# Performance work log

Measured on AMD Instinct MI355X. Metric: run time of the kernel, lower is better.

The kernel has to match this reference:

```python
import jax, jax.numpy as jnp
import numpy as np

N, E, D, H = 50000, 800000, 64, 64  # nodes, edges, in_dim, hid_dim


def setup_inputs() -> dict:
    key = jax.random.key(0)
    ks = jax.random.split(key, 16)
    s = lambda fan_in: 1.0 / np.sqrt(fan_in)
    inp = {
        "node_feat": jax.random.normal(ks[0], (N, D), jnp.float32),
        "coord": jax.random.normal(ks[1], (N, 3), jnp.float32),
        "edge_list": jax.random.randint(ks[2], (E, 2), 0, N, jnp.int32),
        # edge_mlp: Linear(2D+1 -> H), Linear(H -> H)
        "We1": jax.random.normal(ks[3], (2 * D + 1, H), jnp.float32) * s(2 * D + 1),
        "be1": jnp.zeros((H,), jnp.float32),
        "We2": jax.random.normal(ks[4], (H, H), jnp.float32) * s(H),
        "be2": jnp.zeros((H,), jnp.float32),
        # node_mlp: Linear(H+D -> H), Linear(H -> H)
        "Wn1": jax.random.normal(ks[5], (H + D, H), jnp.float32) * s(H + D),
        "bn1": jnp.zeros((H,), jnp.float32),
        "Wn2": jax.random.normal(ks[6], (H, H), jnp.float32) * s(H),
        "bn2": jnp.zeros((H,), jnp.float32),
        # coord_mlp: Linear(H -> H), Linear(H -> 1, bias=False, xavier gain 1e-3)
        "Wc1": jax.random.normal(ks[7], (H, H), jnp.float32) * s(H),
        "bc1": jnp.zeros((H,), jnp.float32),
        "wc": jax.random.normal(ks[8], (H, 1), jnp.float32) * 0.001,
    }
    return inp


def reference(node_feat, coord, edge_list, We1, be1, We2, be2,
              Wn1, bn1, Wn2, bn2, Wc1, bc1, wc):
    n = node_feat.shape[0]
    node_in = edge_list[:, 0]
    node_out = edge_list[:, 1]

    # coord2radial (normalize=False)
    coord_diff = coord[node_out] - coord[node_in]            # [E,3]
    radial = jnp.sum(coord_diff * coord_diff, axis=1, keepdims=True)  # [E,1]

    # edge_function (no edge_attr, no attention)
    edge_in = jnp.concatenate(
        [node_feat[node_in], node_feat[node_out], radial], axis=1)    # [E,2D+1]
    h = jax.nn.relu(edge_in @ We1 + be1)
    edge_feat = jax.nn.relu(h @ We2 + be2)                   # [E,H]

    # coord_function, coords_agg='mean'
    trans_w = jax.nn.relu(edge_feat @ Wc1 + bc1) @ wc        # [E,1]
    weighted_trans = coord_diff * trans_w                    # [E,3]
    agg = jax.ops.segment_sum(weighted_trans, node_out, num_segments=n)
    cnt = jax.ops.segment_sum(jnp.ones((node_out.shape[0],), coord.dtype),
                              node_out, num_segments=n)
    coord_out = coord + agg / jnp.maximum(cnt, 1.0)[:, None]

    # node_function (residual, dims match)
    agg_edge = jax.ops.segment_sum(edge_feat, node_out, num_segments=n)  # [N,H]
    node_in_feat = jnp.concatenate([node_feat, agg_edge], axis=1)
    nf = jax.nn.relu(node_in_feat @ Wn1 + bn1) @ Wn2 + bn2
    node_feat_out = node_feat + nf

    return node_feat_out, coord_out
```

## Files before the change

kernel.cpp:

```cpp
#include <hip/hip_runtime.h>

#define NN 50000
#define NE 800000
#define PREP_BLOCKS 784
#define PREP_THREADS (PREP_BLOCKS * 256)

typedef __bf16 bf16x8 __attribute__((ext_vector_type(8)));
typedef float  f32x4  __attribute__((ext_vector_type(4)));

__device__ __forceinline__ float frelu(float x) { return fmaxf(x, 0.f); }

__global__ __launch_bounds__(256) void prep_kernel(
    const float* __restrict__ nf, const int* __restrict__ el,
    const float* __restrict__ We1, const float* __restrict__ We2,
    const float* __restrict__ Wc1, const float* __restrict__ Wn1,
    const float* __restrict__ Wn2, const float* __restrict__ be1,
    __bf16* __restrict__ W2T,  __bf16* __restrict__ Wc1T,
    __bf16* __restrict__ Wn1T, __bf16* __restrict__ Wn2T,
    __bf16* __restrict__ Pa, __bf16* __restrict__ Pb,
    int* __restrict__ deg, int* __restrict__ rank, float* __restrict__ agg_edge,
    int* __restrict__ counter)
{
    __shared__ __align__(16) __bf16 w1lds[64 * 128];
    if (blockIdx.x < 196) {
        for (int idx = threadIdx.x; idx < 64 * 128; idx += 256) {
            const int k = idx >> 6;
            const int j = idx & 63;
            w1lds[j * 128 + (k ^ ((j & 7) << 3))] = (__bf16)We1[k * 64 + j];
        }
    }

    const int tid = blockIdx.x * 256 + threadIdx.x;
    if (tid == 0) *counter = 0;

    if (tid < 4096) {
        const int j = tid & 63, k = tid >> 6;
        W2T [j * 64 + k] = (__bf16)We2[k * 64 + j];
        Wc1T[j * 64 + k] = (__bf16)Wc1[k * 64 + j];
        Wn2T[j * 64 + k] = (__bf16)Wn2[k * 64 + j];
        Wn1T[j * 128 + k]      = (__bf16)Wn1[k * 64 + j];
        Wn1T[j * 128 + 64 + k] = (__bf16)Wn1[(64 + k) * 64 + j];
    }

    {
        const f32x4 z = (f32x4){0.f, 0.f, 0.f, 0.f};
        for (int i = tid; i < NN * 16; i += PREP_THREADS)
            ((f32x4*)agg_edge)[i] = z;
    }

    for (int e = tid; e < NE; e += PREP_THREADS) {
        const int2 pr = ((const int2*)el)[e];
        rank[e] = atomicAdd(&deg[pr.y], 1);
    }

    if (blockIdx.x >= 196) return;
    __syncthreads();

    const int w = threadIdx.x >> 6, lane = threadIdx.x & 63;
    const int c = lane & 15, g = lane >> 4;
    const int mbase = blockIdx.x * 256 + w * 64;

    bf16x8 af[4][2];
#pragma unroll
    for (int m = 0; m < 4; ++m) {
        int node = mbase + m * 16 + c;
        node = (node < NN) ? node : (NN - 1);
#pragma unroll
        for (int s = 0; s < 2; ++s) {
            const int k0 = s * 32 + g * 8;
            const float4 v0 = *(const float4*)(nf + (size_t)node * 64 + k0);
            const float4 v1 = *(const float4*)(nf + (size_t)node * 64 + k0 + 4);
            bf16x8 a;
            a[0] = (__bf16)v0.x; a[1] = (__bf16)v0.y; a[2] = (__bf16)v0.z; a[3] = (__bf16)v0.w;
            a[4] = (__bf16)v1.x; a[5] = (__bf16)v1.y; a[6] = (__bf16)v1.z; a[7] = (__bf16)v1.w;
            af[m][s] = a;
        }
    }

    {
        f32x4 cc[4][4];
#pragma unroll
        for (int m = 0; m < 4; ++m)
#pragma unroll
            for (int n = 0; n < 4; ++n) cc[m][n] = (f32x4){0.f, 0.f, 0.f, 0.f};
#pragma unroll
        for (int n = 0; n < 4; ++n)
#pragma unroll
            for (int s = 0; s < 2; ++s) {
                const int j = n * 16 + c;
                const bf16x8 b = *(const bf16x8*)&w1lds[j * 128 + ((s * 32 + g * 8) ^ ((j & 7) << 3))];
#pragma unroll
                for (int m = 0; m < 4; ++m)
                    cc[m][n] = __builtin_amdgcn_mfma_f32_16x16x32_bf16(af[m][s], b, cc[m][n], 0, 0, 0);
            }
#pragma unroll
        for (int m = 0; m < 4; ++m)
#pragma unroll
            for (int n = 0; n < 4; ++n)
#pragma unroll
                for (int r = 0; r < 4; ++r) {
                    const int node = mbase + m * 16 + g * 4 + r;
                    if (node < NN) Pa[(size_t)node * 64 + n * 16 + c] = (__bf16)cc[m][n][r];
                }
    }
    {
        f32x4 cc[4][4];
#pragma unroll
        for (int m = 0; m < 4; ++m)
#pragma unroll
            for (int n = 0; n < 4; ++n) cc[m][n] = (f32x4){0.f, 0.f, 0.f, 0.f};
#pragma unroll
        for (int n = 0; n < 4; ++n)
#pragma unroll
            for (int s = 0; s < 2; ++s) {
                const int j = n * 16 + c;
                const bf16x8 b = *(const bf16x8*)&w1lds[j * 128 + 64 + ((s * 32 + g * 8) ^ ((j & 7) << 3))];
#pragma unroll
                for (int m = 0; m < 4; ++m)
                    cc[m][n] = __builtin_amdgcn_mfma_f32_16x16x32_bf16(af[m][s], b, cc[m][n], 0, 0, 0);
            }
#pragma unroll
        for (int n = 0; n < 4; ++n) {
            const float bb = be1[n * 16 + c];
#pragma unroll
            for (int m = 0; m < 4; ++m)
#pragma unroll
                for (int r = 0; r < 4; ++r) {
                    const int node = mbase + m * 16 + g * 4 + r;
                    if (node < NN) Pb[(size_t)node * 64 + n * 16 + c] = (__bf16)(cc[m][n][r] + bb);
                }
        }
    }
}

__global__ __launch_bounds__(256) void alloc_kernel(
    const int* __restrict__ deg, int* __restrict__ base, int* __restrict__ counter)
{
    const int n = blockIdx.x * 256 + threadIdx.x;
    const int lid = threadIdx.x & 63;
    const int d = (n < NN) ? deg[n] : 0;
    int pre = d;
#pragma unroll
    for (int off = 1; off < 64; off <<= 1) {
        const int v = __shfl_up(pre, off);
        if (lid >= off) pre += v;
    }
    const int excl = pre - d;
    const int tot = __shfl(pre, 63);
    int wbase = 0;
    if (lid == 63) wbase = atomicAdd(counter, tot);
    wbase = __shfl(wbase, 63);
    if (n < NN) base[n] = wbase + excl;
}

__global__ __launch_bounds__(256) void scatter_kernel(
    const int* __restrict__ el, const int* __restrict__ base,
    const int* __restrict__ rank, int2* __restrict__ sorted_el,
    float* __restrict__ agg3)
{
    const int e = blockIdx.x * 256 + threadIdx.x;
    if (e < NN * 3) agg3[e] = 0.f;
    const int2 pr = ((const int2*)el)[e];
    sorted_el[base[pr.y] + rank[e]] = pr;
}

__global__ __launch_bounds__(256, 5) void edge_mfma(
    const __bf16* __restrict__ Pa, const __bf16* __restrict__ Pb,
    const float* __restrict__ coord, const int2* __restrict__ sorted_el,
    const float* __restrict__ We1,
    const __bf16* __restrict__ W2T, const float* __restrict__ be2,
    const __bf16* __restrict__ Wc1T, const float* __restrict__ bc1,
    const float* __restrict__ wc,
    float* __restrict__ agg_edge, float* __restrict__ agg3)
{
    __shared__ __align__(16) __bf16 tile[4][64 * 32];
    __shared__ int   nin_s[4][64];
    __shared__ int   nout_s[4][64];
    __shared__ float rad_s[4][64];
    __shared__ float tw_s[4][64];
    __shared__ float cd_s[4][64][3];

    const int w    = threadIdx.x >> 6;
    const int lane = threadIdx.x & 63;
    const int c    = lane & 15;
    const int g    = lane >> 4;
    const int ebase = blockIdx.x * 256 + w * 64;

    const int2 pr = sorted_el[ebase + lane];
    const int nin = pr.x, nout = pr.y;
    nin_s[w][lane]  = nin;
    nout_s[w][lane] = nout;
    const float cdx = coord[3 * nout + 0] - coord[3 * nin + 0];
    const float cdy = coord[3 * nout + 1] - coord[3 * nin + 1];
    const float cdz = coord[3 * nout + 2] - coord[3 * nin + 2];
    rad_s[w][lane] = cdx * cdx + cdy * cdy + cdz * cdz;
    cd_s[w][lane][0] = cdx; cd_s[w][lane][1] = cdy; cd_s[w][lane][2] = cdz;

    bf16x8 af[4][2];
#pragma unroll
    for (int s = 0; s < 2; ++s) {
        const int k0 = s * 32 + g * 8;
        const float4 w1a = *(const float4*)(We1 + 128 * 64 + k0);
        const float4 w1b = *(const float4*)(We1 + 128 * 64 + k0 + 4);
        float wv[8] = {w1a.x, w1a.y, w1a.z, w1a.w, w1b.x, w1b.y, w1b.z, w1b.w};
#pragma unroll
        for (int m = 0; m < 4; ++m) {
            const int e  = m * 16 + c;
            const int ni = nin_s[w][e];
            const int no = nout_s[w][e];
            const float rad = rad_s[w][e];
            const bf16x8 pa = *(const bf16x8*)(Pa + (size_t)ni * 64 + k0);
            const bf16x8 pb = *(const bf16x8*)(Pb + (size_t)no * 64 + k0);
            bf16x8 a;
#pragma unroll
            for (int i = 0; i < 8; ++i)
                a[i] = (__bf16)frelu((float)pa[i] + (float)pb[i] + rad * wv[i]);
            af[m][s] = a;
        }
    }

    bf16x8 a2[4][2];
#pragma unroll
    for (int p = 0; p < 2; ++p) {
        f32x4 c1h[4][2];
#pragma unroll
        for (int q = 0; q < 2; ++q) {
            const float b = be2[(2 * p + q) * 16 + c];
#pragma unroll
            for (int m = 0; m < 4; ++m) c1h[m][q] = (f32x4){b, b, b, b};
        }
#pragma unroll
        for (int q = 0; q < 2; ++q)
#pragma unroll
            for (int s = 0; s < 2; ++s) {
                const bf16x8 b = *(const bf16x8*)(W2T + ((2 * p + q) * 16 + c) * 64 + s * 32 + g * 8);
#pragma unroll
                for (int m = 0; m < 4; ++m)
                    c1h[m][q] = __builtin_amdgcn_mfma_f32_16x16x32_bf16(af[m][s], b, c1h[m][q], 0, 0, 0);
            }

#pragma unroll
        for (int m = 0; m < 4; ++m)
#pragma unroll
            for (int q = 0; q < 2; ++q)
#pragma unroll
                for (int r = 0; r < 4; ++r) {
                    const int e = m * 16 + g * 4 + r;
                    const int lc = q * 16 + c;
                    tile[w][e * 32 + (lc ^ (((e >> 1) & 3) << 3))] = (__bf16)frelu(c1h[m][q][r]);
                }

#pragma unroll
        for (int m = 0; m < 4; ++m) {
            const int e = m * 16 + c;
            a2[m][p] = *(const bf16x8*)&tile[w][e * 32 + ((g * 8) ^ (((e >> 1) & 3) << 3))];
        }

        {
            const int lc = lane & 31;
            const int rbase = (lane >> 5) * 32;
            int cur = nout_s[w][rbase];
            float acc = 0.f;
#pragma unroll 4
            for (int rr = 0; rr < 32; ++rr) {
                const int r = rbase + rr;
                acc += (float)tile[w][r * 32 + (lc ^ (((r >> 1) & 3) << 3))];
                const int nxt = (rr < 31) ? nout_s[w][r + 1] : -1;
                if (nxt != cur) {
                    atomicAdd(&agg_edge[(size_t)cur * 64 + p * 32 + lc], acc);
                    acc = 0.f;
                    cur = nxt;
                }
            }
        }
    }

    f32x4 twp[4];
#pragma unroll
    for (int m = 0; m < 4; ++m) twp[m] = (f32x4){0.f, 0.f, 0.f, 0.f};
#pragma unroll
    for (int n = 0; n < 4; ++n) {
        const float b = bc1[n * 16 + c];
        const float wn = wc[n * 16 + c];
        f32x4 c2[4];
#pragma unroll
        for (int m = 0; m < 4; ++m) c2[m] = (f32x4){b, b, b, b};
#pragma unroll
        for (int s = 0; s < 2; ++s) {
            const bf16x8 bb = *(const bf16x8*)(Wc1T + (n * 16 + c) * 64 + s * 32 + g * 8);
#pragma unroll
            for (int m = 0; m < 4; ++m)
                c2[m] = __builtin_amdgcn_mfma_f32_16x16x32_bf16(a2[m][s], bb, c2[m], 0, 0, 0);
        }
#pragma unroll
        for (int m = 0; m < 4; ++m)
#pragma unroll
            for (int r = 0; r < 4; ++r)
                twp[m][r] = fmaf(frelu(c2[m][r]), wn, twp[m][r]);
    }

#pragma unroll
    for (int m = 0; m < 4; ++m) {
#pragma unroll
        for (int r = 0; r < 4; ++r) {
            float p = twp[m][r];
            p += __shfl_xor(p, 1);
            p += __shfl_xor(p, 2);
            p += __shfl_xor(p, 4);
            p += __shfl_xor(p, 8);
            if (c == 0) tw_s[w][m * 16 + g * 4 + r] = p;
        }
    }

    if (lane < 48) {
        const int dim = lane % 3, chunk = lane / 3;
        const int r0 = chunk * 4;
        int cur = nout_s[w][r0];
        float acc = 0.f;
#pragma unroll
        for (int rr = 0; rr < 4; ++rr) {
            const int r = r0 + rr;
            acc += cd_s[w][r][dim] * tw_s[w][r];
            const int nxt = (rr < 3) ? nout_s[w][r + 1] : -1;
            if (nxt != cur) {
                atomicAdd(&agg3[3 * cur + dim], acc);
                acc = 0.f;
                cur = nxt;
            }
        }
    }
}

__global__ __launch_bounds__(256) void node_mfma(
    const float* __restrict__ nf, const float* __restrict__ coord,
    const float* __restrict__ agg_edge, const int* __restrict__ deg,
    float* agg3_coordout,
    const __bf16* __restrict__ Wn1T, const float* __restrict__ bn1,
    const __bf16* __restrict__ Wn2T, const float* __restrict__ bn2,
    float* __restrict__ out_feat)
{
    __shared__ __align__(16) __bf16 tile[4][64 * 64];
    const int t = threadIdx.x;
    const int w = t >> 6, lane = t & 63, c = lane & 15, g = lane >> 4;
    const int nblk = blockIdx.x * 256;

    const int nodeT = nblk + t;
    if (nodeT < NN) {
        const float invc = 1.f / fmaxf((float)deg[nodeT], 1.f);
#pragma unroll
        for (int d = 0; d < 3; ++d) {
            const float a = agg3_coordout[3 * nodeT + d];
            agg3_coordout[3 * nodeT + d] = coord[3 * nodeT + d] + a * invc;
        }
    }

    const int mbase = nblk + w * 64;

    bf16x8 a1[4][4];
#pragma unroll
    for (int m = 0; m < 4; ++m) {
        int node = mbase + m * 16 + c;
        node = (node < NN) ? node : (NN - 1);
#pragma unroll
        for (int s = 0; s < 4; ++s) {
            const int k0 = s * 32 + g * 8;
            const float* src = (k0 < 64) ? (nf + (size_t)node * 64 + k0)
                                         : (agg_edge + (size_t)node * 64 + (k0 - 64));
            const float4 v0 = *(const float4*)src;
            const float4 v1 = *(const float4*)(src + 4);
            bf16x8 a;
            a[0] = (__bf16)v0.x; a[1] = (__bf16)v0.y; a[2] = (__bf16)v0.z; a[3] = (__bf16)v0.w;
            a[4] = (__bf16)v1.x; a[5] = (__bf16)v1.y; a[6] = (__bf16)v1.z; a[7] = (__bf16)v1.w;
            a1[m][s] = a;
        }
    }

    f32x4 c1[4][4];
#pragma unroll
    for (int n = 0; n < 4; ++n) {
        const float b = bn1[n * 16 + c];
#pragma unroll
        for (int m = 0; m < 4; ++m) c1[m][n] = (f32x4){b, b, b, b};
    }
#pragma unroll
    for (int n = 0; n < 4; ++n)
#pragma unroll
        for (int s = 0; s < 4; ++s) {
            const bf16x8 b = *(const bf16x8*)(Wn1T + (n * 16 + c) * 128 + s * 32 + g * 8);
#pragma unroll
            for (int m = 0; m < 4; ++m)
                c1[m][n] = __builtin_amdgcn_mfma_f32_16x16x32_bf16(a1[m][s], b, c1[m][n], 0, 0, 0);
        }

#pragma unroll
    for (int m = 0; m < 4; ++m)
#pragma unroll
        for (int n = 0; n < 4; ++n)
#pragma unroll
            for (int r = 0; r < 4; ++r) {
                const int e = m * 16 + g * 4 + r;
                tile[w][e * 64 + ((n * 16 + c) ^ ((e & 7) << 3))] = (__bf16)frelu(c1[m][n][r]);
            }

    bf16x8 a2[4][2];
#pragma unroll
    for (int m = 0; m < 4; ++m) {
        const int e = m * 16 + c;
#pragma unroll
        for (int s = 0; s < 2; ++s) {
            const int k0 = s * 32 + g * 8;
            a2[m][s] = *(const bf16x8*)&tile[w][e * 64 + (k0 ^ ((e & 7) << 3))];
        }
    }
    f32x4 c2[4][4];
#pragma unroll
    for (int n = 0; n < 4; ++n) {
        const float b = bn2[n * 16 + c];
#pragma unroll
        for (int m = 0; m < 4; ++m) c2[m][n] = (f32x4){b, b, b, b};
    }
#pragma unroll
    for (int n = 0; n < 4; ++n)
#pragma unroll
        for (int s = 0; s < 2; ++s) {
            const bf16x8 b = *(const bf16x8*)(Wn2T + (n * 16 + c) * 64 + s * 32 + g * 8);
#pragma unroll
            for (int m = 0; m < 4; ++m)
                c2[m][n] = __builtin_amdgcn_mfma_f32_16x16x32_bf16(a2[m][s], b, c2[m][n], 0, 0, 0);
        }

#pragma unroll
    for (int m = 0; m < 4; ++m)
#pragma unroll
        for (int n = 0; n < 4; ++n)
#pragma unroll
            for (int r = 0; r < 4; ++r) {
                const int node = mbase + m * 16 + g * 4 + r;
                if (node < NN) {
                    const int col = n * 16 + c;
                    out_feat[(size_t)node * 64 + col] =
                        nf[(size_t)node * 64 + col] + c2[m][n][r];
                }
            }
}

extern "C" void kernel_launch(void* const* d_in, const int* in_sizes, int n_in,
                              void* d_out, int out_size, void* d_ws, size_t ws_size,
                              hipStream_t stream)
{
    const float* nf    = (const float*)d_in[0];
    const float* coord = (const float*)d_in[1];
    const int*   el    = (const int*)d_in[2];
    const float* We1   = (const float*)d_in[3];
    const float* be1   = (const float*)d_in[4];
    const float* We2   = (const float*)d_in[5];
    const float* be2   = (const float*)d_in[6];
    const float* Wn1   = (const float*)d_in[7];
    const float* bn1   = (const float*)d_in[8];
    const float* Wn2   = (const float*)d_in[9];
    const float* bn2   = (const float*)d_in[10];
    const float* Wc1   = (const float*)d_in[11];
    const float* bc1   = (const float*)d_in[12];
    const float* wc    = (const float*)d_in[13];

    float* out_feat  = (float*)d_out;
    float* out_coord = out_feat + (size_t)NN * 64;

    __bf16* Pa   = (__bf16*)d_out;
    int*    rank = (int*)((char*)d_out + 6400000);
    float*  agg3 = out_coord;

    char* ws = (char*)d_ws;
    __bf16* Pb       = (__bf16*)ws;
    float* agg_edge  = (float*)(ws + 6400000);
    int*   deg       = (int*)(ws + 19200000);
    int*   base      = (int*)(ws + 19400000);
    int2*  sorted_el = (int2*)(ws + 19600000);
    __bf16* W2T  = (__bf16*)(ws + 26000000);
    __bf16* Wc1T = W2T + 4096;
    __bf16* Wn2T = Wc1T + 4096;
    __bf16* Wn1T = Wn2T + 4096;
    int*   counter = (int*)(ws + 26041000);

    hipMemsetAsync(deg, 0, (size_t)NN * sizeof(int), stream);

    prep_kernel<<<dim3(PREP_BLOCKS), dim3(256), 0, stream>>>(
        nf, el, We1, We2, Wc1, Wn1, Wn2, be1,
        W2T, Wc1T, Wn1T, Wn2T,
        Pa, Pb, deg, rank, agg_edge, counter);

    alloc_kernel<<<dim3((NN + 255) / 256), dim3(256), 0, stream>>>(deg, base, counter);

    scatter_kernel<<<dim3(NE / 256), dim3(256), 0, stream>>>(
        el, base, rank, sorted_el, agg3);

    edge_mfma<<<dim3(NE / 256), dim3(256), 0, stream>>>(
        Pa, Pb, coord, sorted_el, We1, W2T, be2, Wc1T, bc1, wc,
        agg_edge, agg3);

    node_mfma<<<dim3((NN + 255) / 256), dim3(256), 0, stream>>>(
        nf, coord, agg_edge, deg, agg3, Wn1T, bn1, Wn2T, bn2, out_feat);
}
```

Before: 195.0 us.

## Replace atomic-counter bucket allocation with deterministic two-level prefix scan

Replaces the per-wave atomicAdd bucket allocation with a block-level scan plus a single-block scan over the 196 chunk sums. Scatter now computes each position as chunk offset plus relative base, so edges come out in true node order rather than an arbitrary wave order. This gives the edge kernel more contiguous destinations, at the cost of one extra small kernel launch and an extra lookup per edge. The edge kernel's launch-bounds occupancy hint is also raised from 5 to 6 waves.

Measured after the change: 256.5 us. 1.32x slower.

```diff
diff --git a/kernel.cpp b/kernel.cpp
--- a/kernel.cpp
+++ b/kernel.cpp
@@ -18,8 +18,7 @@
     __bf16* __restrict__ W2T,  __bf16* __restrict__ Wc1T,
     __bf16* __restrict__ Wn1T, __bf16* __restrict__ Wn2T,
     __bf16* __restrict__ Pa, __bf16* __restrict__ Pb,
-    int* __restrict__ deg, int* __restrict__ rank, float* __restrict__ agg_edge,
-    int* __restrict__ counter)
+    int* __restrict__ deg, int* __restrict__ rank, float* __restrict__ agg_edge)
 {
     __shared__ __align__(16) __bf16 w1lds[64 * 128];
     if (blockIdx.x < 196) {
@@ -31,7 +30,6 @@
     }
 
     const int tid = blockIdx.x * 256 + threadIdx.x;
-    if (tid == 0) *counter = 0;
 
     if (tid < 4096) {
         const int j = tid & 63, k = tid >> 6;
@@ -133,11 +131,14 @@
     }
 }
 
-__global__ __launch_bounds__(256) void alloc_kernel(
-    const int* __restrict__ deg, int* __restrict__ base, int* __restrict__ counter)
-{
-    const int n = blockIdx.x * 256 + threadIdx.x;
-    const int lid = threadIdx.x & 63;
+__global__ __launch_bounds__(256) void alloc1_kernel(
+    const int* __restrict__ deg, int* __restrict__ base_rel,
+    int* __restrict__ chunkSum)
+{
+    __shared__ int wsum[4];
+    const int t = threadIdx.x;
+    const int n = blockIdx.x * 256 + t;
+    const int lid = t & 63, wid = t >> 6;
     const int d = (n < NN) ? deg[n] : 0;
     int pre = d;
 #pragma unroll
@@ -145,26 +146,44 @@
         const int v = __shfl_up(pre, off);
         if (lid >= off) pre += v;
     }
-    const int excl = pre - d;
-    const int tot = __shfl(pre, 63);
-    int wbase = 0;
-    if (lid == 63) wbase = atomicAdd(counter, tot);
-    wbase = __shfl(wbase, 63);
-    if (n < NN) base[n] = wbase + excl;
+    if (lid == 63) wsum[wid] = pre;
+    __syncthreads();
+    int woff = 0;
+#pragma unroll
+    for (int i = 0; i < 4; ++i) if (i < wid) woff += wsum[i];
+    if (n < NN) base_rel[n] = woff + pre - d;
+    if (t == 255) chunkSum[blockIdx.x] = woff + pre;
+}
+
+__global__ __launch_bounds__(256) void alloc2_kernel(
+    const int* __restrict__ chunkSum, int* __restrict__ chunkOff)
+{
+    __shared__ int s[256];
+    const int t = threadIdx.x;
+    const int v0 = (t < 196) ? chunkSum[t] : 0;
+    s[t] = v0;
+    __syncthreads();
+    for (int d = 1; d < 256; d <<= 1) {
+        const int v = (t >= d) ? s[t - d] : 0;
+        __syncthreads();
+        s[t] += v;
+        __syncthreads();
+    }
+    if (t < 196) chunkOff[t] = s[t] - v0;
 }
 
 __global__ __launch_bounds__(256) void scatter_kernel(
-    const int* __restrict__ el, const int* __restrict__ base,
-    const int* __restrict__ rank, int2* __restrict__ sorted_el,
-    float* __restrict__ agg3)
+    const int* __restrict__ el, const int* __restrict__ base_rel,
+    const int* __restrict__ chunkOff, const int* __restrict__ rank,
+    int2* __restrict__ sorted_el, float* __restrict__ agg3)
 {
     const int e = blockIdx.x * 256 + threadIdx.x;
     if (e < NN * 3) agg3[e] = 0.f;
     const int2 pr = ((const int2*)el)[e];
-    sorted_el[base[pr.y] + rank[e]] = pr;
-}
-
-__global__ __launch_bounds__(256, 5) void edge_mfma(
+    sorted_el[chunkOff[pr.y >> 8] + base_rel[pr.y] + rank[e]] = pr;
+}
+
+__global__ __launch_bounds__(256, 6) void edge_mfma(
     const __bf16* __restrict__ Pa, const __bf16* __restrict__ Pb,
     const float* __restrict__ coord, const int2* __restrict__ sorted_el,
     const float* __restrict__ We1,
@@ -474,25 +493,27 @@
     __bf16* Pb       = (__bf16*)ws;
     float* agg_edge  = (float*)(ws + 6400000);
     int*   deg       = (int*)(ws + 19200000);
-    int*   base      = (int*)(ws + 19400000);
+    int*   base_rel  = (int*)(ws + 19400000);
     int2*  sorted_el = (int2*)(ws + 19600000);
     __bf16* W2T  = (__bf16*)(ws + 26000000);
     __bf16* Wc1T = W2T + 4096;
     __bf16* Wn2T = Wc1T + 4096;
     __bf16* Wn1T = Wn2T + 4096;
-    int*   counter = (int*)(ws + 26041000);
+    int*   chunkSum = (int*)(ws + 26041088);
+    int*   chunkOff = (int*)(ws + 26042112);
 
     hipMemsetAsync(deg, 0, (size_t)NN * sizeof(int), stream);
 
     prep_kernel<<<dim3(PREP_BLOCKS), dim3(256), 0, stream>>>(
         nf, el, We1, We2, Wc1, Wn1, Wn2, be1,
         W2T, Wc1T, Wn1T, Wn2T,
-        Pa, Pb, deg, rank, agg_edge, counter);
-
-    alloc_kernel<<<dim3((NN + 255) / 256), dim3(256), 0, stream>>>(deg, base, counter);
+        Pa, Pb, deg, rank, agg_edge);
+
+    alloc1_kernel<<<dim3(196), dim3(256), 0, stream>>>(deg, base_rel, chunkSum);
+    alloc2_kernel<<<dim3(1), dim3(256), 0, stream>>>(chunkSum, chunkOff);
 
     scatter_kernel<<<dim3(NE / 256), dim3(256), 0, stream>>>(
-        el, base, rank, sorted_el, agg3);
+        el, base_rel, chunkOff, rank, sorted_el, agg3);
 
     edge_mfma<<<dim3(NE / 256), dim3(256), 0, stream>>>(
         Pa, Pb, coord, sorted_el, We1, W2T, be2, Wc1T, bc1, wc,
```
